# Kernel tuning notes

Hardware: AMD Instinct MI355X
Metric: run time of the kernel (lower is better)

The kernel has to match this reference:

```python
import jax, jax.numpy as jnp
import numpy as np
import math

G = 8; N0 = 16384; DEG = 8; E = G * N0 * DEG
C = 128; H = 256; OUT = 128; L = 3
RATIO = 0.5; EPS_FA = 0.1


def setup_inputs():
    key = jax.random.key(0)
    ks = jax.random.split(key, 10)
    x = jax.random.normal(ks[0], (G * N0, C), jnp.float32)
    e = jax.random.randint(ks[1], (2, E), 0, N0)
    off = jnp.repeat(jnp.arange(G) * N0, N0 * DEG)  # per-graph node offsets
    edge_index = (e + off[None, :]).astype(jnp.int32)  # (2, E), edges stay within their graph
    batch = jnp.repeat(jnp.arange(G), N0).astype(jnp.int32)
    root = jax.random.normal(ks[2], (G, C), jnp.float32)
    s = 0.05
    att_l = jax.random.normal(ks[3], (L, C), jnp.float32) * s
    att_r = jax.random.normal(ks[4], (L, C), jnp.float32) * s
    w_ih = jax.random.normal(ks[5], (3 * H, C * L), jnp.float32) * s
    w_hh = jax.random.normal(ks[6], (3 * H, H), jnp.float32) * s
    b_ih = jnp.zeros(3 * H, jnp.float32)
    b_hh = jnp.zeros(3 * H, jnp.float32)
    w_fin = jax.random.normal(ks[7], (OUT, H), jnp.float32) * s
    b_fin = jnp.zeros(OUT, jnp.float32)
    w_root = jax.random.normal(ks[8], (OUT, C), jnp.float32) * s
    b_root = jnp.zeros(OUT, jnp.float32)
    residual_alpha = jnp.float32(0.5)
    return dict(x=x, edge_index=edge_index, batch=batch, root=root, att_l=att_l, att_r=att_r,
                w_ih=w_ih, w_hh=w_hh, b_ih=b_ih, b_hh=b_hh, w_fin=w_fin, b_fin=b_fin,
                w_root=w_root, b_root=b_root, residual_alpha=residual_alpha)


def _faconv(xc, x0, src, dst, emask, al_w, ar_w, n):
    # gcn_norm with self-loops: deg over dst (+1 for self loop), w_ij = d_i^-1/2 d_j^-1/2
    deg = jax.ops.segment_sum(emask, dst, num_segments=n) + 1.0
    dinv = jax.lax.rsqrt(deg)
    w = dinv[src] * dinv[dst] * emask
    al = xc @ al_w  # (n,)
    ar = xc @ ar_w
    alpha = jnp.tanh(al[dst] + ar[src])
    out = jax.ops.segment_sum((w * alpha)[:, None] * xc[src], dst, num_segments=n)
    # self-loop message (weight 1/deg_i, alpha = tanh(al_i + ar_i))
    out = out + ((dinv * dinv) * jnp.tanh(al + ar))[:, None] * xc
    return out + EPS_FA * x0


def _forward(x, root, att_l, att_r, w_ih, w_hh, b_ih, b_hh, w_fin, b_fin, w_root, b_root, residual_alpha, edge_index):
    src = edge_index[0]
    dst = edge_index[1]
    emask = jnp.ones(src.shape[0], jnp.float32)  # edge validity mask (replaces dynamic edge filtering)
    cur, orig = x, x
    npg = N0  # nodes per graph at current layer (static)
    outs = []
    for i in range(L):
        n = G * npg
        h = jax.nn.relu(_faconv(cur, orig, src, dst, emask, att_l[i], att_r[i], n))
        outs.append(h.reshape(G, npg, C).max(axis=1))  # global_max_pool per graph
        # ASTGPool: score = out-degree on edge_index[0], per-graph top-k (k = ceil(npg*ratio))
        score = jax.ops.segment_sum(emask, src, num_segments=n)
        k = int(math.ceil(npg * RATIO))
        _, idx = jax.lax.top_k(score.reshape(G, npg), k)
        perm = (idx + (jnp.arange(G) * npg)[:, None]).reshape(-1)  # (G*k,) global kept-node ids
        keep = jnp.zeros(n, bool).at[perm].set(True)
        emask = emask * keep[src].astype(jnp.float32) * keep[dst].astype(jnp.float32)
        nmap = jnp.zeros(n, src.dtype).at[perm].set(jnp.arange(G * k, dtype=src.dtype))
        src, dst = nmap[src], nmap[dst]  # dead edges map to node 0 but have emask==0
        cur, orig, npg = h[perm], orig[perm], k  # multiplier = 1.0
    fused = jnp.concatenate(outs, axis=1)  # (G, C*L)
    # single-step GRU with h0 = 0
    gi = fused @ w_ih.T + b_ih
    ir, iz, inn = jnp.split(gi, 3, axis=1)
    br, bz, bn = jnp.split(b_hh, 3)
    r = jax.nn.sigmoid(ir + br)
    z = jax.nn.sigmoid(iz + bz)
    ncand = jnp.tanh(inn + r * bn)
    hgru = (1.0 - z) * ncand
    gnn_emb = hgru @ w_fin.T + b_fin
    root_emb = root @ w_root.T + b_root
    return residual_alpha * gnn_emb + (1.0 - residual_alpha) * root_emb


def reference(x, edge_index, batch, root, att_l, att_r, w_ih, w_hh, b_ih, b_hh, w_fin, b_fin, w_root, b_root, residual_alpha):
    del batch  # graphs are contiguous equal-size blocks; batch structure is encoded in G, N0
    return _forward(x, root, att_l, att_r, w_ih, w_hh, b_ih, b_hh, w_fin, b_fin, w_root, b_root, residual_alpha, edge_index)
```

## Files before the change

kernel.cpp:

```cpp
#include <hip/hip_runtime.h>
#include <math.h>

#define G 8
#define N0 16384
#define NEDGE (G*N0*8)
#define EPG (NEDGE/G)
#define C 128
#define EPS_FA 0.1f
#define SMAX 2048

typedef unsigned short ushort_t;
typedef unsigned int uint_t;

__device__ inline ushort_t f2bf(float f) {
    uint_t u = __float_as_uint(f);
    uint_t r = (u + 0x7FFFu + ((u >> 16) & 1u)) >> 16;
    return (ushort_t)r;
}
__device__ inline uint_t pack2bf(float a, float b) {
    return (uint_t)f2bf(a) | ((uint_t)f2bf(b) << 16);
}
__device__ inline float bflo(uint_t w) { return __uint_as_float(w << 16); }
__device__ inline float bfhi(uint_t w) { return __uint_as_float(w & 0xFFFF0000u); }

__global__ void __launch_bounds__(256) k_hist0(const int* __restrict__ ei,
                                               unsigned int* __restrict__ bh) {
    __shared__ unsigned int h[N0];
    int t = threadIdx.x;
    for (int i = t; i < N0; i += 256) h[i] = 0;
    __syncthreads();
    int base = blockIdx.x * 8192;
    int gbase = (blockIdx.x >> 4) * N0;
    for (int i = t; i < 8192; i += 256) {
        int s = ei[base + i] - gbase;
        int d = ei[NEDGE + base + i] - gbase;
        atomicAdd(&h[d], 1u);
        atomicAdd(&h[s], 0x10000u);
    }
    __syncthreads();
    unsigned int* o = bh + (size_t)blockIdx.x * N0;
    for (int i = t; i < N0; i += 256) o[i] = h[i];
}

__global__ void k_sumdeg(const unsigned int* __restrict__ bh, int* __restrict__ degI,
                         int* __restrict__ score, int shift, int nsub, int n,
                         float* __restrict__ pooled) {
    int i = blockIdx.x * 256 + threadIdx.x;
    if (pooled && i < G * 384) pooled[i] = 0.0f;
    if (i >= n) return;
    int bins = 1 << shift;
    int g = i >> shift, u = i & (bins - 1);
    const unsigned int* p = bh + ((size_t)(g * nsub) << shift) + u;
    int ad = 0, as = 0;
    for (int b = 0; b < nsub; b++) {
        unsigned int w = p[(size_t)b * bins];
        ad += (int)(w & 0xFFFFu); as += (int)(w >> 16);
    }
    degI[i] = ad; score[i] = as;
}

__global__ void k_alar(const float* __restrict__ x,
                       const float* __restrict__ attl, const float* __restrict__ attr,
                       float* __restrict__ al, float* __restrict__ ar,
                       ushort_t* __restrict__ xb, int n) {
    int wid  = (blockIdx.x * blockDim.x + threadIdx.x) >> 6;
    int lane = threadIdx.x & 63;
    if (wid >= n) return;
    float2 v  = ((const float2*)(x + (size_t)wid * C))[lane];
    ((uint_t*)(xb + (size_t)wid * C))[lane] = pack2bf(v.x, v.y);
    float2 l2 = ((const float2*)attl)[lane];
    float2 r2 = ((const float2*)attr)[lane];
    float sl = v.x * l2.x + v.y * l2.y;
    float sr = v.x * r2.x + v.y * r2.y;
    for (int o = 32; o >= 1; o >>= 1) { sl += __shfl_xor(sl, o); sr += __shfl_xor(sr, o); }
    if (lane == 0) { al[wid] = sl; ar[wid] = sr; }
}

__global__ void __launch_bounds__(256) k_scan1(const int* __restrict__ degI,
                                               int* __restrict__ rowptr,
                                               int* __restrict__ bsum) {
    __shared__ int part[256];
    int t = threadIdx.x;
    int base = blockIdx.x * 2048 + t * 8;
    int v[8]; int s = 0;
    for (int i = 0; i < 8; i++) { v[i] = degI[base + i]; s += v[i]; }
    part[t] = s; __syncthreads();
    for (int o = 1; o < 256; o <<= 1) {
        int val = part[t];
        int add = (t >= o) ? part[t - o] : 0;
        __syncthreads();
        part[t] = val + add;
        __syncthreads();
    }
    int run = (t == 0) ? 0 : part[t - 1];
    if (t == 255) bsum[blockIdx.x] = part[255];
    for (int i = 0; i < 8; i++) { rowptr[base + i] = run; run += v[i]; }
}

__global__ void k_scan3s(int* __restrict__ rowptr, int* __restrict__ cursor,
                         const int* __restrict__ bsum, const int* __restrict__ degI,
                         const float* __restrict__ al, const float* __restrict__ ar,
                         float* __restrict__ dinv, float* __restrict__ selfco,
                         unsigned char* __restrict__ keep, int* __restrict__ nmap, int n) {
    __shared__ int base_s;
    int t = threadIdx.x;
    if (t < 64) {
        int c = blockIdx.x >> 3;
        int vv = (t < c) ? bsum[t] : 0;
        for (int o = 32; o >= 1; o >>= 1) vv += __shfl_xor(vv, o);
        if (t == 0) base_s = vv;
    }
    __syncthreads();
    int i = blockIdx.x * 256 + t;
    if (i >= n) return;
    int v = rowptr[i] + base_s;
    rowptr[i] = v; cursor[i] = v;
    float d  = (float)degI[i] + 1.0f;
    float di = rsqrtf(d);
    dinv[i]   = di;
    selfco[i] = di * di * tanhf(al[i] + ar[i]);
    keep[i] = 0; nmap[i] = 0;
}

__global__ void k_fill(const int* __restrict__ src, const int* __restrict__ dst,
                       const unsigned char* __restrict__ em,
                       const float* __restrict__ dinv, const float* __restrict__ al,
                       const float* __restrict__ ar,
                       int* __restrict__ cursor, int2* __restrict__ edges) {
    int gph = blockIdx.x & 7;
    int chunk = blockIdx.x >> 3;
    int e = gph * EPG + chunk * 256 + threadIdx.x;
    if (em && !em[e]) return;
    int s = src[e], d = dst[e];
    float cf = dinv[s] * dinv[d] * tanhf(al[d] + ar[s]);
    int pos = atomicAdd(&cursor[d], 1);
    edges[pos] = make_int2(s, __float_as_int(cf));
}

#define ACC4(W, CF) { a0 += (CF) * bflo((W).x); a1 += (CF) * bfhi((W).x); \
                      a2 += (CF) * bflo((W).y); a3 += (CF) * bfhi((W).y); }
__global__ void __launch_bounds__(256) k_msg_csr(
        const int* __restrict__ rowptr, const int* __restrict__ degI,
        const int2* __restrict__ edges,
        const ushort_t* __restrict__ cur, const ushort_t* __restrict__ xb,
        const int* __restrict__ oidx, const float* __restrict__ selfco,
        ushort_t* __restrict__ h, float* __restrict__ pb, int npg) {
    __shared__ float pm[8 * 128];
    int g    = blockIdx.x & 7;
    int ib   = blockIdx.x >> 3;
    int sub  = threadIdx.x >> 5;
    int lane = threadIdx.x & 31;
    int v = g * npg + ib * 8 + sub;
    int rs = rowptr[v], deg = degI[v];
    int o = oidx ? oidx[v] : v;
    uint2 cw = ((const uint2*)(cur + (size_t)v * C))[lane];
    uint2 xw = ((const uint2*)(xb  + (size_t)o * C))[lane];
    float sc = selfco[v];
    float a0 = 0.0f, a1 = 0.0f, a2 = 0.0f, a3 = 0.0f;
    for (int j0 = 0; j0 < deg; j0 += 32) {
        int cnt = deg - j0; if (cnt > 32) cnt = 32;
        int2 er = make_int2(0, 0);
        if (lane < cnt) er = edges[rs + j0 + lane];
        uint2 w0 = make_uint2(0,0), w1 = w0, w2 = w0, w3 = w0;
        {
            int s0 = __shfl(er.x, 0, 32);
            if (0 < cnt) w0 = ((const uint2*)(cur + (size_t)s0 * C))[lane];
            int s1 = __shfl(er.x, 1, 32);
            if (1 < cnt) w1 = ((const uint2*)(cur + (size_t)s1 * C))[lane];
            int s2 = __shfl(er.x, 2, 32);
            if (2 < cnt) w2 = ((const uint2*)(cur + (size_t)s2 * C))[lane];
            int s3 = __shfl(er.x, 3, 32);
            if (3 < cnt) w3 = ((const uint2*)(cur + (size_t)s3 * C))[lane];
        }
        int j = 0;
        for (; j + 4 <= cnt; j += 4) {
            float cf0 = __int_as_float(__shfl(er.y, j, 32));
            ACC4(w0, cf0);
            int sn0 = __shfl(er.x, j + 4, 32);
            if (j + 4 < cnt) w0 = ((const uint2*)(cur + (size_t)sn0 * C))[lane];
            float cf1 = __int_as_float(__shfl(er.y, j + 1, 32));
            ACC4(w1, cf1);
            int sn1 = __shfl(er.x, j + 5, 32);
            if (j + 5 < cnt) w1 = ((const uint2*)(cur + (size_t)sn1 * C))[lane];
            float cf2 = __int_as_float(__shfl(er.y, j + 2, 32));
            ACC4(w2, cf2);
            int sn2 = __shfl(er.x, j + 6, 32);
            if (j + 6 < cnt) w2 = ((const uint2*)(cur + (size_t)sn2 * C))[lane];
            float cf3 = __int_as_float(__shfl(er.y, j + 3, 32));
            ACC4(w3, cf3);
            int sn3 = __shfl(er.x, j + 7, 32);
            if (j + 7 < cnt) w3 = ((const uint2*)(cur + (size_t)sn3 * C))[lane];
        }
        if (j < cnt)     { float cf = __int_as_float(__shfl(er.y, j,     32)); ACC4(w0, cf); }
        if (j + 1 < cnt) { float cf = __int_as_float(__shfl(er.y, j + 1, 32)); ACC4(w1, cf); }
        if (j + 2 < cnt) { float cf = __int_as_float(__shfl(er.y, j + 2, 32)); ACC4(w2, cf); }
    }
    float r0 = fmaxf(a0 + sc * bflo(cw.x) + EPS_FA * bflo(xw.x), 0.0f);
    float r1 = fmaxf(a1 + sc * bfhi(cw.x) + EPS_FA * bfhi(xw.x), 0.0f);
    float r2 = fmaxf(a2 + sc * bflo(cw.y) + EPS_FA * bflo(xw.y), 0.0f);
    float r3 = fmaxf(a3 + sc * bfhi(cw.y) + EPS_FA * bfhi(xw.y), 0.0f);
    uint2 hw; hw.x = pack2bf(r0, r1); hw.y = pack2bf(r2, r3);
    ((uint2*)(h + (size_t)v * C))[lane] = hw;
    float4 rr = make_float4(r0, r1, r2, r3);
    ((float4*)(pm + sub * 128))[lane] = rr;
    __syncthreads();
    int t = threadIdx.x;
    if (t < 128) {
        float m = pm[t];
        for (int s = 1; s < 8; s++) m = fmaxf(m, pm[s * 128 + t]);
        pb[(size_t)blockIdx.x * 128 + t] = m;
    }
}

__global__ void __launch_bounds__(256) k_poolred(const float* __restrict__ pb,
                                                 float* __restrict__ pooled, int layer) {
    __shared__ float sm[256];
    int g = blockIdx.x & 7;
    int ch = blockIdx.x >> 3;
    int t = threadIdx.x;
    int c = t & 127, half = t >> 7;
    float m = 0.0f;
    for (int i = 0; i < 32; i++) {
        int r = ch * 64 + half * 32 + i;
        m = fmaxf(m, pb[(size_t)(g + 8 * r) * 128 + c]);
    }
    sm[t] = m;
    __syncthreads();
    if (t < 128) {
        float mm = fmaxf(sm[t], sm[t + 128]);
        atomicMax((unsigned int*)&pooled[g * 384 + layer * 128 + c], __float_as_uint(mm));
    }
}

__global__ void __launch_bounds__(256) k_hist(const int* __restrict__ score, int npg, int nb,
                                              int* __restrict__ blockhist) {
    __shared__ int lh[SMAX];
    int g = blockIdx.x / nb, b = blockIdx.x % nb, t = threadIdx.x;
    for (int s = t; s < SMAX; s += 256) lh[s] = 0;
    __syncthreads();
    int s = score[g * npg + b * 256 + t];
    if (s > SMAX - 1) s = SMAX - 1;
    atomicAdd(&lh[s], 1);
    __syncthreads();
    int* outp = blockhist + ((size_t)g * nb + b) * SMAX;
    for (int i = t; i < SMAX; i += 256) outp[i] = lh[i];
}

__global__ void __launch_bounds__(256) k_binprefix(int* __restrict__ blockhist,
                                                   int* __restrict__ hist, int nb) {
    __shared__ int tile[64 * 256];
    int g = blockIdx.x >> 3, ch = blockIdx.x & 7, t = threadIdx.x;
    int s0 = ch * 256;
    int* bg = blockhist + (size_t)g * nb * SMAX + s0;
    for (int b = 0; b < nb; b++) tile[b * 256 + t] = bg[(size_t)b * SMAX + t];
    __syncthreads();
    int acc = 0;
    for (int b = 0; b < nb; b++) {
        int v = tile[b * 256 + t];
        tile[b * 256 + t] = acc;
        acc += v;
    }
    __syncthreads();
    for (int b = 0; b < nb; b++) bg[(size_t)b * SMAX + t] = tile[b * 256 + t];
    hist[g * SMAX + s0 + t] = acc;
}

__global__ void __launch_bounds__(256) k_rank(const int* __restrict__ score,
                                              const int* __restrict__ blockhist,
                                              const int* __restrict__ hist,
                                              int npg, int nb, int k,
                                              unsigned char* __restrict__ keep,
                                              int* __restrict__ nmap, int* __restrict__ perm) {
    __shared__ int bp[SMAX];
    __shared__ int part[256];
    __shared__ int cs[256];
    int g = blockIdx.x / nb, b = blockIdx.x % nb, t = threadIdx.x;
    const int* hg = hist + g * SMAX;
    int v[8]; int sm = 0;
    for (int i = 0; i < 8; i++) { v[i] = hg[SMAX - 1 - (t * 8 + i)]; sm += v[i]; }
    part[t] = sm; __syncthreads();
    for (int o = 1; o < 256; o <<= 1) {
        int val = part[t];
        int add = (t >= o) ? part[t - o] : 0;
        __syncthreads();
        part[t] = val + add;
        __syncthreads();
    }
    int run = (t == 0) ? 0 : part[t - 1];
    for (int i = 0; i < 8; i++) { bp[SMAX - 1 - (t * 8 + i)] = run; run += v[i]; }
    int vv = b * 256 + t;
    int s = score[g * npg + vv];
    if (s > SMAX - 1) s = SMAX - 1;
    cs[t] = s;
    __syncthreads();
    int cnt = 0;
    for (int u = 0; u < t; u++) cnt += (cs[u] == s);
    int pos = bp[s] + blockhist[((size_t)g * nb + b) * SMAX + s] + cnt;
    if (pos < k) {
        int vg = g * npg + vv;
        int nid = g * k + pos;
        keep[vg] = 1; nmap[vg] = nid; perm[nid] = vg;
    }
}

__global__ void k_gather_alar(const ushort_t* __restrict__ h, const int* __restrict__ perm,
                              const int* __restrict__ oidx,
                              const float* __restrict__ attlN, const float* __restrict__ attrN,
                              ushort_t* __restrict__ curN, int* __restrict__ oidxN,
                              float* __restrict__ al, float* __restrict__ ar, int m) {
    int i = blockIdx.x * 256 + threadIdx.x;
    if (i >= m * 32) return;
    int j = i >> 5, c4 = i & 31;
    int p = perm[j];
    uint2 w = ((const uint2*)(h + (size_t)p * C))[c4];
    ((uint2*)(curN + (size_t)j * C))[c4] = w;
    float f0 = bflo(w.x), f1 = bfhi(w.x), f2 = bflo(w.y), f3 = bfhi(w.y);
    float4 l4 = ((const float4*)attlN)[c4];
    float4 r4 = ((const float4*)attrN)[c4];
    float sl = f0 * l4.x + f1 * l4.y + f2 * l4.z + f3 * l4.w;
    float sr = f0 * r4.x + f1 * r4.y + f2 * r4.z + f3 * r4.w;
    for (int o = 16; o >= 1; o >>= 1) { sl += __shfl_xor(sl, o); sr += __shfl_xor(sr, o); }
    if (c4 == 0) {
        al[j] = sl; ar[j] = sr;
        oidxN[j] = oidx ? oidx[p] : p;
    }
}

__global__ void __launch_bounds__(256) k_remap_hist(
        const int* __restrict__ inS, const int* __restrict__ inD,
        const unsigned char* __restrict__ inEm,
        int* __restrict__ src, int* __restrict__ dst, unsigned char* __restrict__ em,
        const unsigned char* __restrict__ keep, const int* __restrict__ nmap,
        unsigned int* __restrict__ bh, int kN) {
    __shared__ unsigned int h[8192];
    int t = threadIdx.x;
    for (int i = t; i < kN; i += 256) h[i] = 0;
    __syncthreads();
    int base = blockIdx.x * 4096;
    int gb = (blockIdx.x >> 5) * kN;
    for (int i = t; i < 4096; i += 256) {
        int e = base + i;
        int s = inS[e], d = inD[e];
        bool ok = (!inEm || inEm[e]) && keep[s] && keep[d];
        if (ok) {
            int ns = nmap[s], nd = nmap[d];
            src[e] = ns; dst[e] = nd; em[e] = 1;
            atomicAdd(&h[nd - gb], 1u);
            atomicAdd(&h[ns - gb], 0x10000u);
        } else { src[e] = 0; dst[e] = 0; em[e] = 0; }
    }
    __syncthreads();
    unsigned int* o = bh + (size_t)blockIdx.x * kN;
    for (int i = t; i < kN; i += 256) o[i] = h[i];
}

__global__ void __launch_bounds__(256) k_gi(const float* __restrict__ pooled,
                                            const float* __restrict__ wih,
                                            const float* __restrict__ bih,
                                            float* __restrict__ gi) {
    int g = blockIdx.y;
    int row = blockIdx.x * 4 + (threadIdx.x >> 6);
    int lane = threadIdx.x & 63;
    const float* w = wih + (size_t)row * 384;
    const float* f = pooled + g * 384;
    float s = 0.0f;
    #pragma unroll
    for (int i = 0; i < 6; i++) s += w[i * 64 + lane] * f[i * 64 + lane];
    for (int o = 32; o >= 1; o >>= 1) s += __shfl_xor(s, o);
    if (lane == 0) gi[g * 768 + row] = s + bih[row];
}

__global__ void __launch_bounds__(256) k_gru_fin(const float* __restrict__ gi,
        const float* __restrict__ bhh, const float* __restrict__ wfin,
        const float* __restrict__ bfin, const float* __restrict__ wroot,
        const float* __restrict__ broot, const float* __restrict__ rootv,
        const float* __restrict__ alphap, float* __restrict__ out) {
    int g = blockIdx.x, t = threadIdx.x;
    __shared__ float hg[256];
    {
        float r  = 1.0f / (1.0f + expf(-(gi[g * 768 + t]       + bhh[t])));
        float z  = 1.0f / (1.0f + expf(-(gi[g * 768 + 256 + t] + bhh[256 + t])));
        float nc = tanhf(gi[g * 768 + 512 + t] + r * bhh[512 + t]);
        hg[t] = (1.0f - z) * nc;
    }
    __syncthreads();
    float a = alphap[0];
    int wv = t >> 6, lane = t & 63;
    const float* rg = rootv + (size_t)g * 128;
    for (int oo = 0; oo < 32; oo++) {
        int o = wv * 32 + oo;
        const float* wf = wfin + (size_t)o * 256;
        float sf = wf[lane] * hg[lane] + wf[64 + lane] * hg[64 + lane]
                 + wf[128 + lane] * hg[128 + lane] + wf[192 + lane] * hg[192 + lane];
        const float* wr = wroot + (size_t)o * 128;
        float sr = wr[lane] * rg[lane] + wr[64 + lane] * rg[64 + lane];
        float s = a * sf + (1.0f - a) * sr;
        for (int sh = 32; sh >= 1; sh >>= 1) s += __shfl_xor(s, sh);
        if (lane == 0)
            out[g * 128 + o] = s + a * bfin[o] + (1.0f - a) * broot[o];
    }
}

extern "C" void kernel_launch(void* const* d_in, const int* in_sizes, int n_in,
                              void* d_out, int out_size, void* d_ws, size_t ws_size,
                              hipStream_t stream) {
    const float* x      = (const float*)d_in[0];
    const int*   ei     = (const int*)d_in[1];
    const float* rootv  = (const float*)d_in[3];
    const float* att_l  = (const float*)d_in[4];
    const float* att_r  = (const float*)d_in[5];
    const float* w_ih   = (const float*)d_in[6];
    const float* b_ih   = (const float*)d_in[8];
    const float* b_hh   = (const float*)d_in[9];
    const float* w_fin  = (const float*)d_in[10];
    const float* b_fin  = (const float*)d_in[11];
    const float* w_root = (const float*)d_in[12];
    const float* b_root = (const float*)d_in[13];
    const float* alphap = (const float*)d_in[14];
    float* out = (float*)d_out;

    char* wsb = (char*)d_ws;
    size_t off = 0;
    auto alloc = [&](size_t bytes) -> char* {
        char* p = wsb + off; off += (bytes + 255) & ~(size_t)255; return p;
    };
    ushort_t* xb   = (ushort_t*)alloc((size_t)131072 * C * 2);
    ushort_t* bufH = (ushort_t*)alloc((size_t)131072 * C * 2);
    ushort_t* bufC = (ushort_t*)alloc((size_t)65536  * C * 2);
    int*   srcA   = (int*)alloc((size_t)NEDGE * 4);
    int*   dstA   = (int*)alloc((size_t)NEDGE * 4);
    unsigned char* emask = (unsigned char*)alloc(NEDGE);
    int2*  edges  = (int2*)alloc((size_t)NEDGE * 8);
    float* al     = (float*)alloc(131072 * 4);
    float* ar     = (float*)alloc(131072 * 4);
    float* dinv   = (float*)alloc(131072 * 4);
    float* selfco = (float*)alloc(131072 * 4);
    int*   degI   = (int*)alloc(131072 * 4);
    int*   score  = (int*)alloc(131072 * 4);
    int*   rowptr = (int*)alloc(131072 * 4);
    int*   cursor = (int*)alloc(131072 * 4);
    int*   bsum   = (int*)alloc(256 * 4);
    unsigned char* keep = (unsigned char*)alloc(131072);
    int*   nmap   = (int*)alloc(131072 * 4);
    int*   perm   = (int*)alloc(65536 * 4);
    int*   oidxA  = (int*)alloc(65536 * 4);
    int*   oidxB  = (int*)alloc(32768 * 4);
    float* pooled = (float*)alloc(G * 384 * 4);
    float* giBuf  = (float*)alloc(G * 768 * 4);
    int*   blockhist = (int*)alloc((size_t)G * 64 * SMAX * 4);
    int*   histT  = (int*)alloc((size_t)G * SMAX * 4);
    unsigned int* bh = (unsigned int*)alloc((size_t)128 * N0 * 4);
    float* pb = (float*)bh;

    k_hist0<<<128, 256, 0, stream>>>(ei, bh);
    k_sumdeg<<<131072 / 256, 256, 0, stream>>>(bh, degI, score, 14, 16, 131072, pooled);

    const int ns[3]   = {131072, 65536, 32768};
    const int npgs[3] = {16384, 8192, 4096};
    const int ks[3]   = {8192, 4096, 0};
    const int shifts[3] = {14, 13, 12};

    for (int l = 0; l < 3; l++) {
        int n = ns[l], npg = npgs[l], k = ks[l];
        const ushort_t* cur = (l == 0) ? xb : bufC;
        const int* oidx = (l == 0) ? nullptr : (l == 1 ? oidxA : oidxB);
        int* oidxN = (l == 0) ? oidxA : oidxB;
        const int* eS = (l == 0) ? ei : srcA;
        const int* eD = (l == 0) ? ei + NEDGE : dstA;
        const unsigned char* eM = (l == 0) ? nullptr : emask;

        if (l == 0)
            k_alar<<<n / 4, 256, 0, stream>>>(x, att_l, att_r, al, ar, xb, n);

        int nblk = n / 2048;
        k_scan1<<<nblk, 256, 0, stream>>>(degI, rowptr, bsum);
        k_scan3s<<<n / 256, 256, 0, stream>>>(rowptr, cursor, bsum, degI, al, ar,
                                              dinv, selfco, keep, nmap, n);

        k_fill<<<NEDGE / 256, 256, 0, stream>>>(eS, eD, eM, dinv, al, ar,
                                                cursor, edges);
        k_msg_csr<<<n / 8, 256, 0, stream>>>(rowptr, degI, edges, cur, xb, oidx,
                                             selfco, bufH, pb, npg);
        k_poolred<<<npg / 64, 256, 0, stream>>>(pb, pooled, l);

        if (l < 2) {
            int nb = npg / 256;
            k_hist<<<G * nb, 256, 0, stream>>>(score, npg, nb, blockhist);
            k_binprefix<<<G * 8, 256, 0, stream>>>(blockhist, histT, nb);
            k_rank<<<G * nb, 256, 0, stream>>>(score, blockhist, histT, npg, nb, k,
                                               keep, nmap, perm);
            int m = G * k;
            k_gather_alar<<<(m * 32 + 255) / 256, 256, 0, stream>>>(
                bufH, perm, oidx, att_l + (l + 1) * C, att_r + (l + 1) * C,
                bufC, oidxN, al, ar, m);
            k_remap_hist<<<256, 256, 0, stream>>>(eS, eD, eM, srcA, dstA, emask,
                                                  keep, nmap, bh, k);
            k_sumdeg<<<(G * k + 255) / 256, 256, 0, stream>>>(bh, degI, score,
                                                              shifts[l + 1], 32, G * k,
                                                              nullptr);
        }
    }

    k_gi<<<dim3(192, G), 256, 0, stream>>>(pooled, w_ih, b_ih, giBuf);
    k_gru_fin<<<G, 256, 0, stream>>>(giBuf, b_hh, w_fin, b_fin, w_root, b_root,
                                     rootv, alphap, out);
}
```

Before: 457.0 us.

## Replace atomic cursor CSR fill with precomputed per-block ranks and prefixes

The histogram kernels now record each edge's local rank within its destination bin from the shared-memory atomic's return value. The degree-summing kernel converts the per-block histograms in place into exclusive prefixes across sub-blocks. The fill kernel then computes each edge's CSR slot as rowptr + block prefix + local rank, so the global atomicAdd on a cursor array and the cursor buffer go away. This costs an extra 16-bit rank write and read per edge plus a scattered read of the block prefix. Slot order also becomes deterministic.

```diff
diff --git a/kernel.cpp b/kernel.cpp
--- a/kernel.cpp
+++ b/kernel.cpp
@@ -24,7 +24,8 @@
 __device__ inline float bfhi(uint_t w) { return __uint_as_float(w & 0xFFFF0000u); }
 
 __global__ void __launch_bounds__(256) k_hist0(const int* __restrict__ ei,
-                                               unsigned int* __restrict__ bh) {
+                                               unsigned int* __restrict__ bh,
+                                               ushort_t* __restrict__ lrank) {
     __shared__ unsigned int h[N0];
     int t = threadIdx.x;
     for (int i = t; i < N0; i += 256) h[i] = 0;
@@ -34,7 +35,8 @@
     for (int i = t; i < 8192; i += 256) {
         int s = ei[base + i] - gbase;
         int d = ei[NEDGE + base + i] - gbase;
-        atomicAdd(&h[d], 1u);
+        unsigned int old = atomicAdd(&h[d], 1u);
+        lrank[base + i] = (ushort_t)(old & 0xFFFFu);
         atomicAdd(&h[s], 0x10000u);
     }
     __syncthreads();
@@ -42,7 +44,7 @@
     for (int i = t; i < N0; i += 256) o[i] = h[i];
 }
 
-__global__ void k_sumdeg(const unsigned int* __restrict__ bh, int* __restrict__ degI,
+__global__ void k_sumdeg(unsigned int* __restrict__ bh, int* __restrict__ degI,
                          int* __restrict__ score, int shift, int nsub, int n,
                          float* __restrict__ pooled) {
     int i = blockIdx.x * 256 + threadIdx.x;
@@ -50,13 +52,14 @@
     if (i >= n) return;
     int bins = 1 << shift;
     int g = i >> shift, u = i & (bins - 1);
-    const unsigned int* p = bh + ((size_t)(g * nsub) << shift) + u;
-    int ad = 0, as = 0;
+    unsigned int* p = bh + ((size_t)(g * nsub) << shift) + u;
+    unsigned int run = 0; int as = 0;
     for (int b = 0; b < nsub; b++) {
         unsigned int w = p[(size_t)b * bins];
-        ad += (int)(w & 0xFFFFu); as += (int)(w >> 16);
-    }
-    degI[i] = ad; score[i] = as;
+        p[(size_t)b * bins] = run;
+        run += w & 0xFFFFu; as += (int)(w >> 16);
+    }
+    degI[i] = (int)run; score[i] = as;
 }
 
 __global__ void k_alar(const float* __restrict__ x,
@@ -97,7 +100,7 @@
     for (int i = 0; i < 8; i++) { rowptr[base + i] = run; run += v[i]; }
 }
 
-__global__ void k_scan3s(int* __restrict__ rowptr, int* __restrict__ cursor,
+__global__ void k_scan3s(int* __restrict__ rowptr,
                          const int* __restrict__ bsum, const int* __restrict__ degI,
                          const float* __restrict__ al, const float* __restrict__ ar,
                          float* __restrict__ dinv, float* __restrict__ selfco,
@@ -113,8 +116,7 @@
     __syncthreads();
     int i = blockIdx.x * 256 + t;
     if (i >= n) return;
-    int v = rowptr[i] + base_s;
-    rowptr[i] = v; cursor[i] = v;
+    rowptr[i] += base_s;
     float d  = (float)degI[i] + 1.0f;
     float di = rsqrtf(d);
     dinv[i]   = di;
@@ -126,15 +128,21 @@
                        const unsigned char* __restrict__ em,
                        const float* __restrict__ dinv, const float* __restrict__ al,
                        const float* __restrict__ ar,
-                       int* __restrict__ cursor, int2* __restrict__ edges) {
+                       const int* __restrict__ rowptr,
+                       const unsigned int* __restrict__ bpre,
+                       const ushort_t* __restrict__ lrank,
+                       int2* __restrict__ edges,
+                       int ebShift, int nsubShift, int binShift) {
     int gph = blockIdx.x & 7;
     int chunk = blockIdx.x >> 3;
     int e = gph * EPG + chunk * 256 + threadIdx.x;
     if (em && !em[e]) return;
     int s = src[e], d = dst[e];
     float cf = dinv[s] * dinv[d] * tanhf(al[d] + ar[s]);
-    int pos = atomicAdd(&cursor[d], 1);
-    edges[pos] = make_int2(s, __float_as_int(cf));
+    int b = e >> ebShift;
+    int gb = (b >> nsubShift) << binShift;
+    int slot = rowptr[d] + (int)bpre[((size_t)b << binShift) + (d - gb)] + (int)lrank[e];
+    edges[slot] = make_int2(s, __float_as_int(cf));
 }
 
 #define ACC4(W, CF) { a0 += (CF) * bflo((W).x); a1 += (CF) * bfhi((W).x); \
@@ -331,7 +339,7 @@
         const unsigned char* __restrict__ inEm,
         int* __restrict__ src, int* __restrict__ dst, unsigned char* __restrict__ em,
         const unsigned char* __restrict__ keep, const int* __restrict__ nmap,
-        unsigned int* __restrict__ bh, int kN) {
+        unsigned int* __restrict__ bh, ushort_t* __restrict__ lrank, int kN) {
     __shared__ unsigned int h[8192];
     int t = threadIdx.x;
     for (int i = t; i < kN; i += 256) h[i] = 0;
@@ -345,7 +353,8 @@
         if (ok) {
             int ns = nmap[s], nd = nmap[d];
             src[e] = ns; dst[e] = nd; em[e] = 1;
-            atomicAdd(&h[nd - gb], 1u);
+            unsigned int old = atomicAdd(&h[nd - gb], 1u);
+            lrank[e] = (ushort_t)(old & 0xFFFFu);
             atomicAdd(&h[ns - gb], 0x10000u);
         } else { src[e] = 0; dst[e] = 0; em[e] = 0; }
     }
@@ -431,6 +440,7 @@
     int*   dstA   = (int*)alloc((size_t)NEDGE * 4);
     unsigned char* emask = (unsigned char*)alloc(NEDGE);
     int2*  edges  = (int2*)alloc((size_t)NEDGE * 8);
+    ushort_t* lrank = (ushort_t*)alloc((size_t)NEDGE * 2);
     float* al     = (float*)alloc(131072 * 4);
     float* ar     = (float*)alloc(131072 * 4);
     float* dinv   = (float*)alloc(131072 * 4);
@@ -438,7 +448,6 @@
     int*   degI   = (int*)alloc(131072 * 4);
     int*   score  = (int*)alloc(131072 * 4);
     int*   rowptr = (int*)alloc(131072 * 4);
-    int*   cursor = (int*)alloc(131072 * 4);
     int*   bsum   = (int*)alloc(256 * 4);
     unsigned char* keep = (unsigned char*)alloc(131072);
     int*   nmap   = (int*)alloc(131072 * 4);
@@ -452,7 +461,7 @@
     unsigned int* bh = (unsigned int*)alloc((size_t)128 * N0 * 4);
     float* pb = (float*)bh;
 
-    k_hist0<<<128, 256, 0, stream>>>(ei, bh);
+    k_hist0<<<128, 256, 0, stream>>>(ei, bh, lrank);
     k_sumdeg<<<131072 / 256, 256, 0, stream>>>(bh, degI, score, 14, 16, 131072, pooled);
 
     const int ns[3]   = {131072, 65536, 32768};
@@ -468,17 +477,21 @@
         const int* eS = (l == 0) ? ei : srcA;
         const int* eD = (l == 0) ? ei + NEDGE : dstA;
         const unsigned char* eM = (l == 0) ? nullptr : emask;
+        int ebShift   = (l == 0) ? 13 : 12;
+        int nsubShift = (l == 0) ? 4  : 5;
+        int binShift  = shifts[l];
 
         if (l == 0)
             k_alar<<<n / 4, 256, 0, stream>>>(x, att_l, att_r, al, ar, xb, n);
 
         int nblk = n / 2048;
         k_scan1<<<nblk, 256, 0, stream>>>(degI, rowptr, bsum);
-        k_scan3s<<<n / 256, 256, 0, stream>>>(rowptr, cursor, bsum, degI, al, ar,
+        k_scan3s<<<n / 256, 256, 0, stream>>>(rowptr, bsum, degI, al, ar,
                                               dinv, selfco, keep, nmap, n);
 
         k_fill<<<NEDGE / 256, 256, 0, stream>>>(eS, eD, eM, dinv, al, ar,
-                                                cursor, edges);
+                                                rowptr, bh, lrank, edges,
+                                                ebShift, nsubShift, binShift);
         k_msg_csr<<<n / 8, 256, 0, stream>>>(rowptr, degI, edges, cur, xb, oidx,
                                              selfco, bufH, pb, npg);
         k_poolred<<<npg / 64, 256, 0, stream>>>(pb, pooled, l);
@@ -494,7 +507,7 @@
                 bufH, perm, oidx, att_l + (l + 1) * C, att_r + (l + 1) * C,
                 bufC, oidxN, al, ar, m);
             k_remap_hist<<<256, 256, 0, stream>>>(eS, eD, eM, srcA, dstA, emask,
-                                                  keep, nmap, bh, k);
+                                                  keep, nmap, bh, lrank, k);
             k_sumdeg<<<(G * k + 255) / 256, 256, 0, stream>>>(bh, degI, score,
                                                               shifts[l + 1], 32, G * k,
                                                               nullptr);
```

After: 438.9 us. 4.0% less time.
